# Kernel optimization log

Hardware: AMD Instinct MI355X
Metric: run time of the kernel (lower is better)

The kernel has to match this reference:

```python
import jax, jax.numpy as jnp
import numpy as np

B, MAXLEN, F, D = 1024, 200, 64, 64
NEG_PAD = -2.0**32 + 1.0  # tf.ones_like(a) * (-2**32 + 1)


def setup_inputs() -> dict:
    key = jax.random.key(0)
    ks = jax.random.split(key, 9)
    return {
        "q": jax.random.normal(ks[0], (B, F, D), jnp.float32),
        "k": jax.random.normal(ks[1], (B, MAXLEN, D), jnp.float32),
        "v": jax.random.normal(ks[2], (B, MAXLEN, D), jnp.float32),
        "kes_length": jax.random.randint(ks[3], (B, 1), 0, MAXLEN, dtype=jnp.int32),
        "field_strengths": jax.random.normal(ks[4], (F, 1), jnp.float32) * 0.05,
        "bias": jax.random.normal(ks[5], (1,), jnp.float32) * 0.05,
        "W_query": jax.random.normal(ks[6], (D, D), jnp.float32) * 0.05,
        "W_key": jax.random.normal(ks[7], (D, D), jnp.float32) * 0.05,
        "W_value": jax.random.normal(ks[8], (D, D), jnp.float32) * 0.05,
    }


def reference(q, k, v, kes_length, field_strengths, bias, W_query, W_key, W_value):
    # is_keys_diff=True branch: project q/k, and v comes from projected k
    qp = jnp.einsum('bfd,de->bfe', q, W_query)   # [B,F,D]
    vp = jnp.einsum('btd,de->bte', k, W_value)   # [B,T,D]
    kp = jnp.einsum('btd,de->bte', k, W_key)     # [B,T,D]

    # Original: tile q->[B,T,F,D], k->[B,T,F,D], a=q*k*fs, sum over F (+bias),
    # then sum over D.  Fused: score[b,t] = sum_d (sum_f qp[b,f,d]*fs[f]) * kp[b,t,d]
    # and the +bias inside [B,T,D] then sum over D contributes bias*D.
    fs = field_strengths[:, 0]                   # [F]
    qw = jnp.einsum('bfd,f->bd', qp, fs)         # field-weighted query, [B,D]
    score = jnp.einsum('bd,btd->bt', qw, kp) + bias[0] * D  # [B,T]

    a = jax.nn.sigmoid(score)
    mask = jnp.arange(MAXLEN)[None, :] < kes_length[:, :1]  # sequence_mask, [B,T]
    a = jnp.where(mask, a, jnp.float32(NEG_PAD))
    a = a / jnp.sqrt(jnp.float32(D))             # / emb_dim**0.5 (after masking, as in source)
    a = jax.nn.softmax(a, axis=-1)               # weight_softmax=True

    out = jnp.einsum('bt,btd->bd', a, vp)        # [B,1,T] @ [B,T,D]
    return out[:, None, :]                       # [B,1,D]
```

## Files before the change

kernel.cpp:

```cpp
#include <hip/hip_runtime.h>
#include <math.h>


namespace {
constexpr int MAXLEN = 200;
constexpr int DD     = 64;

__device__ __forceinline__ void load_lds16(const float* g, float* l) {
    __builtin_amdgcn_global_load_lds(
        (const __attribute__((address_space(1))) void*)g,
        (__attribute__((address_space(3))) void*)l,
        16, 0, 0);
}

__global__ __launch_bounds__(256, 4)
void auto_attn_kernel(const float* __restrict__ q,
                      const float* __restrict__ k,
                      const int*   __restrict__ kes_length,
                      const float* __restrict__ fs,
                      const float* __restrict__ bias,
                      const float* __restrict__ Wq,
                      const float* __restrict__ Wk,
                      const float* __restrict__ Wv,
                      float*       __restrict__ out)
{
    __shared__ float kt[MAXLEN * DD];
    __shared__ float red[256];
    __shared__ float vec[DD];
    __shared__ float qks[DD];
    __shared__ float sw[MAXLEN];
    __shared__ float sS[4];

    const int tid  = threadIdx.x;
    const int b    = blockIdx.x;
    const int lane = tid & 63;
    const int wave = tid >> 6;

    const float* kb = k + (size_t)b * (MAXLEN * DD);
    const float* qb = q + (size_t)b * (DD * DD);

    for (int j = wave; j < 50; j += 4)
        load_lds16(kb + j * 256 + lane * 4, &kt[j * 256]);

    const int len = kes_length[b];

    float acc = 0.f;
    #pragma unroll
    for (int i = 0; i < 16; ++i) {
        const int f = wave * 16 + i;
        acc += fs[f] * qb[f * 64 + lane];
    }
    red[tid] = acc;
    __syncthreads();
    if (tid < 64) vec[tid] = red[tid] + red[tid + 64] + red[tid + 128] + red[tid + 192];
    __syncthreads();

    acc = 0.f;
    #pragma unroll
    for (int i = 0; i < 16; ++i) {
        const int dd = wave * 16 + i;
        acc += vec[dd] * Wq[dd * 64 + lane];
    }
    red[tid] = acc;
    __syncthreads();
    if (tid < 64) vec[tid] = red[tid] + red[tid + 64] + red[tid + 128] + red[tid + 192];
    __syncthreads();

    acc = 0.f;
    #pragma unroll
    for (int i = 0; i < 16; ++i) {
        const int e = wave * 16 + i;
        acc += Wk[lane * 64 + e] * vec[e];
    }
    red[tid] = acc;
    __syncthreads();
    if (tid < 64) qks[tid] = red[tid] + red[tid + 64] + red[tid + 128] + red[tid + 192];
    __syncthreads();

    const float bscale = bias[0] * 64.0f;
    const int t = tid;
    if (t < MAXLEN) {
        float s = 0.f;
        #pragma unroll
        for (int i = 0; i < 64; ++i) {
            const int idx = (i + lane) & 63;
            s += kt[t * 64 + idx] * qks[idx];
        }
        s += bscale;
        float w;
        if (len == 0)      w = 1.0f;
        else if (t < len) { const float sig = 1.0f / (1.0f + __expf(-s));
                            w = __expf(sig * 0.125f); }
        else               w = 0.0f;
        sw[t] = w;
    }
    __syncthreads();

    float kacc = 0.f, Sr = 0.f;
    #pragma unroll 10
    for (int i = 0; i < 50; ++i) {
        const int t2 = wave * 50 + i;
        const float w = sw[t2];
        kacc += w * kt[t2 * 64 + lane];
        Sr   += w;
    }
    red[tid] = kacc;
    if (lane == 0) sS[wave] = Sr;
    __syncthreads();
    if (tid < 64) {
        const float S = sS[0] + sS[1] + sS[2] + sS[3];
        vec[tid] = (red[tid] + red[tid + 64] + red[tid + 128] + red[tid + 192]) / S;
    }
    __syncthreads();

    acc = 0.f;
    #pragma unroll
    for (int i = 0; i < 16; ++i) {
        const int dd = wave * 16 + i;
        acc += vec[dd] * Wv[dd * 64 + lane];
    }
    red[tid] = acc;
    __syncthreads();
    if (tid < 64)
        out[(size_t)b * 64 + tid] = red[tid] + red[tid + 64] + red[tid + 128] + red[tid + 192];
}
}

extern "C" void kernel_launch(void* const* d_in, const int* in_sizes, int n_in,
                              void* d_out, int out_size, void* d_ws, size_t ws_size,
                              hipStream_t stream) {
    const float* q    = (const float*)d_in[0];
    const float* k    = (const float*)d_in[1];
    const int*   kes  = (const int*)  d_in[3];
    const float* fs   = (const float*)d_in[4];
    const float* bias = (const float*)d_in[5];
    const float* Wq   = (const float*)d_in[6];
    const float* Wk   = (const float*)d_in[7];
    const float* Wv   = (const float*)d_in[8];
    float* out = (float*)d_out;

    auto_attn_kernel<<<dim3(1024), dim3(256), 0, stream>>>(q, k, kes, fs, bias, Wq, Wk, Wv, out);
}
```

Measured before the change: 142.4 us.

## Stream K rows through registers instead of staging all of K in LDS

Drops the 51KB LDS copy of the per-batch K tile. Each group of four threads now owns one token at a time, holds 16 columns in registers, and prefetches the next 64-token chunk while computing. The score dot product is reduced with lane shuffles, and the weighted sum of K is accumulated in registers, then reduced through a small padded LDS scratch. This cuts LDS footprint so more blocks can be resident per CU and removes LDS read traffic, at the cost of more registers and an extra reduction stage.

```diff
diff --git a/kernel.cpp b/kernel.cpp
--- a/kernel.cpp
+++ b/kernel.cpp
@@ -4,14 +4,6 @@
 
 namespace {
 constexpr int MAXLEN = 200;
-constexpr int DD     = 64;
-
-__device__ __forceinline__ void load_lds16(const float* g, float* l) {
-    __builtin_amdgcn_global_load_lds(
-        (const __attribute__((address_space(1))) void*)g,
-        (__attribute__((address_space(3))) void*)l,
-        16, 0, 0);
-}
 
 __global__ __launch_bounds__(256, 4)
 void auto_attn_kernel(const float* __restrict__ q,
@@ -24,24 +16,27 @@
                       const float* __restrict__ Wv,
                       float*       __restrict__ out)
 {
-    __shared__ float kt[MAXLEN * DD];
     __shared__ float red[256];
-    __shared__ float vec[DD];
-    __shared__ float qks[DD];
-    __shared__ float sw[MAXLEN];
+    __shared__ float vec[64];
+    __shared__ float qks[64];
+    __shared__ float scr[64 * 65];
     __shared__ float sS[4];
 
     const int tid  = threadIdx.x;
     const int b    = blockIdx.x;
     const int lane = tid & 63;
     const int wave = tid >> 6;
+    const int tok  = tid >> 2;
+    const int dq   = (tid & 3) << 4;
 
-    const float* kb = k + (size_t)b * (MAXLEN * DD);
-    const float* qb = q + (size_t)b * (DD * DD);
+    const float* kb = k + (size_t)b * (MAXLEN * 64);
+    const float* qb = q + (size_t)b * (64 * 64);
 
-    for (int j = wave; j < 50; j += 4)
-        load_lds16(kb + j * 256 + lane * 4, &kt[j * 256]);
-
+    float4 cur[4], nxt[4];
+    {
+        const float4* kr = (const float4*)(kb + tok * 64 + dq);
+        cur[0] = kr[0]; cur[1] = kr[1]; cur[2] = kr[2]; cur[3] = kr[3];
+    }
     const int len = kes_length[b];
 
     float acc = 0.f;
@@ -77,40 +72,76 @@
     if (tid < 64) qks[tid] = red[tid] + red[tid + 64] + red[tid + 128] + red[tid + 192];
     __syncthreads();
 
+    float qkreg[16];
+    {
+        const float4* qp = (const float4*)(qks + dq);
+        #pragma unroll
+        for (int j = 0; j < 4; ++j) {
+            const float4 t4 = qp[j];
+            qkreg[j*4+0] = t4.x; qkreg[j*4+1] = t4.y;
+            qkreg[j*4+2] = t4.z; qkreg[j*4+3] = t4.w;
+        }
+    }
+
     const float bscale = bias[0] * 64.0f;
-    const int t = tid;
-    if (t < MAXLEN) {
+
+    float kacc[16];
+    #pragma unroll
+    for (int i = 0; i < 16; ++i) kacc[i] = 0.f;
+    float Sr = 0.f;
+
+    #pragma unroll
+    for (int c = 0; c < 4; ++c) {
+        if (c < 3) {
+            const int tn = (c + 1) * 64 + tok;
+            if (tn < MAXLEN) {
+                const float4* kr = (const float4*)(kb + tn * 64 + dq);
+                nxt[0] = kr[0]; nxt[1] = kr[1]; nxt[2] = kr[2]; nxt[3] = kr[3];
+            }
+        }
+        const int t = c * 64 + tok;
+        const float* cf = (const float*)cur;
         float s = 0.f;
         #pragma unroll
-        for (int i = 0; i < 64; ++i) {
-            const int idx = (i + lane) & 63;
-            s += kt[t * 64 + idx] * qks[idx];
+        for (int i = 0; i < 16; ++i) s += cf[i] * qkreg[i];
+        s += __shfl_xor(s, 1);
+        s += __shfl_xor(s, 2);
+        s += bscale;
+        float w = 0.f;
+        if (t < MAXLEN) {
+            if (len == 0)      w = 1.0f;
+            else if (t < len) { const float sig = 1.0f / (1.0f + __expf(-s));
+                                w = __expf(sig * 0.125f); }
         }
-        s += bscale;
-        float w;
-        if (len == 0)      w = 1.0f;
-        else if (t < len) { const float sig = 1.0f / (1.0f + __expf(-s));
-                            w = __expf(sig * 0.125f); }
-        else               w = 0.0f;
-        sw[t] = w;
+        #pragma unroll
+        for (int i = 0; i < 16; ++i) kacc[i] += w * cf[i];
+        Sr += w;
+        if (c < 3) {
+            cur[0] = nxt[0]; cur[1] = nxt[1]; cur[2] = nxt[2]; cur[3] = nxt[3];
+        }
     }
+
+    float Sw = Sr;
+    Sw += __shfl_xor(Sw, 4);
+    Sw += __shfl_xor(Sw, 8);
+    Sw += __shfl_xor(Sw, 16);
+    Sw += __shfl_xor(Sw, 32);
+    if (lane == 0) sS[wave] = Sw;
+
+    #pragma unroll
+    for (int i = 0; i < 16; ++i) scr[tok * 65 + dq + i] = kacc[i];
     __syncthreads();
-
-    float kacc = 0.f, Sr = 0.f;
-    #pragma unroll 10
-    for (int i = 0; i < 50; ++i) {
-        const int t2 = wave * 50 + i;
-        const float w = sw[t2];
-        kacc += w * kt[t2 * 64 + lane];
-        Sr   += w;
+    const float S = sS[0] + sS[1] + sS[2] + sS[3];
+    acc = 0.f;
+    #pragma unroll
+    for (int i = 0; i < 16; ++i) {
+        const int row = wave * 16 + i;
+        acc += scr[row * 65 + lane];
     }
-    red[tid] = kacc;
-    if (lane == 0) sS[wave] = Sr;
+    red[tid] = acc;
     __syncthreads();
-    if (tid < 64) {
-        const float S = sS[0] + sS[1] + sS[2] + sS[3];
+    if (tid < 64)
         vec[tid] = (red[tid] + red[tid + 64] + red[tid + 128] + red[tid + 192]) / S;
-    }
     __syncthreads();
 
     acc = 0.f;
```

After: 140.3 us. Within noise of the previous version (-1.5%).
